# Performance work log

Hardware: AMD Instinct MI355X
Metric: run time of the kernel (lower is better)

Reference implementation:

```python
import jax, jax.numpy as jnp
import numpy as np

B, S = 256, 16384
HUBER_DELTA = 1.0  # torch.nn.HuberLoss default


def setup_inputs() -> dict:
    key = jax.random.key(0)
    k1, k2, k3 = jax.random.split(key, 3)
    pred_coords = jax.random.normal(k1, (B, S, 3), dtype=jnp.float32)
    target_coords = jax.random.normal(k2, (B, S, 3), dtype=jnp.float32)
    mask = jax.random.randint(k3, (B, S), 0, 2).astype(jnp.int32)
    return {"pred_coords": pred_coords, "target_coords": target_coords, "mask": mask}


def _kabsch_align(pred, target, maskf):
    # pred/target: [B,S,3], maskf: [B,S] (0/1). Batched masked Kabsch.
    cnt = maskf.sum(axis=1, keepdims=True)                      # [B,1]
    cp = (pred * maskf[..., None]).sum(axis=1) / cnt            # [B,3] pred center
    ct = (target * maskf[..., None]).sum(axis=1) / cnt          # [B,3] target center
    pc = (pred - cp[:, None, :]) * maskf[..., None]             # masked centered pred
    tc = target - ct[:, None, :]                                # centered target
    H = jnp.einsum('bsi,bsj->bij', pc, tc)                      # [B,3,3] covariance
    U, _, Vt = jnp.linalg.svd(H)                                # batched 3x3 SVD
    R = jnp.einsum('bji,bkj->bik', Vt, U)                       # Vt^T @ U^T
    sign = jnp.where(jnp.linalg.det(R) < 0, -1.0, 1.0)          # [B] reflection fix
    flip = jnp.ones((pred.shape[0], 3), dtype=pred.dtype).at[:, -1].set(sign)
    Vt = Vt * flip[:, :, None]                                  # flip last row of Vt
    R = jnp.einsum('bji,bkj->bik', Vt, U)
    t = ct - jnp.einsum('bij,bj->bi', R, cp)                    # [B,3]
    aligned = jnp.einsum('bij,bsj->bsi', R, pred) + t[:, None, :]
    return aligned


def _huber(d):
    a = jnp.abs(d)
    return jnp.where(a < HUBER_DELTA, 0.5 * d * d, HUBER_DELTA * (a - 0.5 * HUBER_DELTA))


def reference(pred_coords, target_coords, mask):
    maskf = mask.astype(pred_coords.dtype)                      # [B,S]
    aligned = _kabsch_align(pred_coords, target_coords, maskf)  # [B,S,3]
    # (torch computes a clamped coord_diff here but never uses it in the loss)
    loss = _huber(aligned - target_coords) * maskf[..., None]   # [B,S,3]
    return loss.sum() / maskf.sum()
```

## Files before the change

### kernel.cpp

```cpp
#include <hip/hip_runtime.h>


#define NB 256
#define NS 16384
#define TPB 256
#define PPT 4
#define CHUNKS (NS / (TPB * PPT))

__device__ __forceinline__ float wave_sum(float v) {
#pragma unroll
    for (int o = 32; o > 0; o >>= 1) v += __shfl_xor(v, o, 64);
    return v;
}

__device__ __forceinline__ float huber(float d) {
    float a = fabsf(d);
    return a < 1.f ? 0.5f * d * d : a - 0.5f;
}

__global__ __launch_bounds__(TPB) void reduce_kernel(
    const float* __restrict__ pred, const float* __restrict__ tgt,
    const int* __restrict__ mask, float* __restrict__ part)
{
    const int b = blockIdx.y, j = blockIdx.x, tid = threadIdx.x;
    const long base = (long)b * NS + (long)(j * TPB + tid) * PPT;
    const float4* p4 = reinterpret_cast<const float4*>(pred + base * 3);
    const float4* t4 = reinterpret_cast<const float4*>(tgt + base * 3);
    const int4 m4 = *reinterpret_cast<const int4*>(mask + base);
    float4 pA = p4[0], pB = p4[1], pC = p4[2];
    float4 tA = t4[0], tB = t4[1], tC = t4[2];
    float P[4][3] = {{pA.x,pA.y,pA.z},{pA.w,pB.x,pB.y},{pB.z,pB.w,pC.x},{pC.y,pC.z,pC.w}};
    float T[4][3] = {{tA.x,tA.y,tA.z},{tA.w,tB.x,tB.y},{tB.z,tB.w,tC.x},{tC.y,tC.z,tC.w}};
    float m[4] = {(float)m4.x,(float)m4.y,(float)m4.z,(float)m4.w};

    float acc[16];
#pragma unroll
    for (int i = 0; i < 16; ++i) acc[i] = 0.f;
#pragma unroll
    for (int k = 0; k < PPT; ++k) {
        const float mk = m[k];
        const float mp0 = mk * P[k][0], mp1 = mk * P[k][1], mp2 = mk * P[k][2];
        acc[0] += mk;
        acc[1] += mp0;            acc[2] += mp1;            acc[3] += mp2;
        acc[4] += mk * T[k][0];   acc[5] += mk * T[k][1];   acc[6] += mk * T[k][2];
        acc[7]  += mp0 * T[k][0]; acc[8]  += mp0 * T[k][1]; acc[9]  += mp0 * T[k][2];
        acc[10] += mp1 * T[k][0]; acc[11] += mp1 * T[k][1]; acc[12] += mp1 * T[k][2];
        acc[13] += mp2 * T[k][0]; acc[14] += mp2 * T[k][1]; acc[15] += mp2 * T[k][2];
    }
#pragma unroll
    for (int i = 0; i < 16; ++i) acc[i] = wave_sum(acc[i]);

    __shared__ float red[4][16];
    const int wave = tid >> 6, lane = tid & 63;
    if (lane == 0) {
#pragma unroll
        for (int i = 0; i < 16; ++i) red[wave][i] = acc[i];
    }
    __syncthreads();
    if (tid < 16) {
        part[((b * CHUNKS + j) << 4) + tid] =
            red[0][tid] + red[1][tid] + red[2][tid] + red[3][tid];
    }
}

__global__ __launch_bounds__(NB) void svd_kernel(
    const float* __restrict__ part, float* __restrict__ RT)
{
    const int b = threadIdx.x;
    const float4* p4 = reinterpret_cast<const float4*>(part);
    float a[16];
#pragma unroll
    for (int i = 0; i < 16; ++i) a[i] = 0.f;
    for (int k = 0; k < CHUNKS; ++k) {
        const int row = (b * CHUNKS + k) << 2;
        float4 v0 = p4[row], v1 = p4[row+1], v2 = p4[row+2], v3 = p4[row+3];
        a[0]+=v0.x;  a[1]+=v0.y;  a[2]+=v0.z;  a[3]+=v0.w;
        a[4]+=v1.x;  a[5]+=v1.y;  a[6]+=v1.z;  a[7]+=v1.w;
        a[8]+=v2.x;  a[9]+=v2.y;  a[10]+=v2.z; a[11]+=v2.w;
        a[12]+=v3.x; a[13]+=v3.y; a[14]+=v3.z; a[15]+=v3.w;
    }
    const float cnt = a[0];
    const float inv = 1.f / cnt;
    const float cpx=a[1]*inv, cpy=a[2]*inv, cpz=a[3]*inv;
    const float ctx=a[4]*inv, cty=a[5]*inv, ctz=a[6]*inv;
    const float Sxx = a[7]  - cnt*cpx*ctx;
    const float Sxy = a[8]  - cnt*cpx*cty;
    const float Sxz = a[9]  - cnt*cpx*ctz;
    const float Syx = a[10] - cnt*cpy*ctx;
    const float Syy = a[11] - cnt*cpy*cty;
    const float Syz = a[12] - cnt*cpy*ctz;
    const float Szx = a[13] - cnt*cpz*ctx;
    const float Szy = a[14] - cnt*cpz*cty;
    const float Szz = a[15] - cnt*cpz*ctz;
    const float N00 =  Sxx + Syy + Szz;
    const float N01 =  Syz - Szy;
    const float N02 =  Szx - Sxz;
    const float N03 =  Sxy - Syx;
    const float N11 =  Sxx - Syy - Szz;
    const float N12 =  Sxy + Syx;
    const float N13 =  Szx + Sxz;
    const float N22 = -Sxx + Syy - Szz;
    const float N23 =  Syz + Szy;
    const float N33 = -Sxx - Syy + Szz;
    const float fro = sqrtf(N00*N00 + N11*N11 + N22*N22 + N33*N33 +
                2.f*(N01*N01 + N02*N02 + N03*N03 + N12*N12 + N13*N13 + N23*N23));
    const float sh = fro + 1e-20f;

    float qw = 1.f, qx = 0.1f, qy = 0.2f, qz = 0.3f;
    for (int it = 0; it < 160; ++it) {
        float nw = N00*qw + N01*qx + N02*qy + N03*qz + sh*qw;
        float nx = N01*qw + N11*qx + N12*qy + N13*qz + sh*qx;
        float ny = N02*qw + N12*qx + N22*qy + N23*qz + sh*qy;
        float nz = N03*qw + N13*qx + N23*qy + N33*qz + sh*qz;
        if ((it & 3) == 3) {
            const float r = rsqrtf(nw*nw + nx*nx + ny*ny + nz*nz);
            nw *= r; nx *= r; ny *= r; nz *= r;
        }
        qw = nw; qx = nx; qy = ny; qz = nz;
    }
    {
        const float r = rsqrtf(qw*qw + qx*qx + qy*qy + qz*qz);
        qw *= r; qx *= r; qy *= r; qz *= r;
    }
    const float R00 = 1.f - 2.f*(qy*qy + qz*qz);
    const float R01 = 2.f*(qx*qy - qw*qz);
    const float R02 = 2.f*(qx*qz + qw*qy);
    const float R10 = 2.f*(qx*qy + qw*qz);
    const float R11 = 1.f - 2.f*(qx*qx + qz*qz);
    const float R12 = 2.f*(qy*qz - qw*qx);
    const float R20 = 2.f*(qx*qz - qw*qy);
    const float R21 = 2.f*(qy*qz + qw*qx);
    const float R22 = 1.f - 2.f*(qx*qx + qy*qy);
    const float tx = ctx - (R00*cpx + R01*cpy + R02*cpz);
    const float ty = cty - (R10*cpx + R11*cpy + R12*cpz);
    const float tz = ctz - (R20*cpx + R21*cpy + R22*cpz);
    float* o = RT + b * 16;
    o[0]=R00; o[1]=R01; o[2]=R02; o[3]=R10; o[4]=R11; o[5]=R12;
    o[6]=R20; o[7]=R21; o[8]=R22; o[9]=tx; o[10]=ty; o[11]=tz; o[12]=cnt;
}

__global__ __launch_bounds__(TPB) void loss_kernel(
    const float* __restrict__ pred, const float* __restrict__ tgt,
    const int* __restrict__ mask, const float* __restrict__ RT,
    float* __restrict__ lpart)
{
    const int b = blockIdx.y, j = blockIdx.x, tid = threadIdx.x;
    __shared__ float C[12];
    if (tid < 12) C[tid] = RT[b * 16 + tid];
    __syncthreads();
    const long base = (long)b * NS + (long)(j * TPB + tid) * PPT;
    const float4* p4 = reinterpret_cast<const float4*>(pred + base * 3);
    const float4* t4 = reinterpret_cast<const float4*>(tgt + base * 3);
    const int4 m4 = *reinterpret_cast<const int4*>(mask + base);
    float4 pA = p4[0], pB = p4[1], pC = p4[2];
    float4 tA = t4[0], tB = t4[1], tC = t4[2];
    float P[4][3] = {{pA.x,pA.y,pA.z},{pA.w,pB.x,pB.y},{pB.z,pB.w,pC.x},{pC.y,pC.z,pC.w}};
    float T[4][3] = {{tA.x,tA.y,tA.z},{tA.w,tB.x,tB.y},{tB.z,tB.w,tC.x},{tC.y,tC.z,tC.w}};
    float m[4] = {(float)m4.x,(float)m4.y,(float)m4.z,(float)m4.w};

    float ls = 0.f;
#pragma unroll
    for (int k = 0; k < PPT; ++k) {
        const float ax = C[0]*P[k][0] + C[1]*P[k][1] + C[2]*P[k][2] + C[9];
        const float ay = C[3]*P[k][0] + C[4]*P[k][1] + C[5]*P[k][2] + C[10];
        const float az = C[6]*P[k][0] + C[7]*P[k][1] + C[8]*P[k][2] + C[11];
        ls += m[k] * (huber(ax - T[k][0]) + huber(ay - T[k][1]) + huber(az - T[k][2]));
    }
    ls = wave_sum(ls);
    __shared__ float red[4];
    const int wave = tid >> 6, lane = tid & 63;
    if (lane == 0) red[wave] = ls;
    __syncthreads();
    if (tid == 0) lpart[b * CHUNKS + j] = red[0] + red[1] + red[2] + red[3];
}

__global__ __launch_bounds__(NB) void final_kernel(
    const float* __restrict__ lpart, const float* __restrict__ RT,
    float* __restrict__ out)
{
    const int tid = threadIdx.x;
    float ls = 0.f;
#pragma unroll
    for (int k = 0; k < CHUNKS; ++k) ls += lpart[tid + NB * k];
    float cs = RT[tid * 16 + 12];
    ls = wave_sum(ls);
    cs = wave_sum(cs);
    __shared__ float rl[4], rc[4];
    const int wave = tid >> 6, lane = tid & 63;
    if (lane == 0) { rl[wave] = ls; rc[wave] = cs; }
    __syncthreads();
    if (tid == 0)
        out[0] = (rl[0]+rl[1]+rl[2]+rl[3]) / (rc[0]+rc[1]+rc[2]+rc[3]);
}

extern "C" void kernel_launch(void* const* d_in, const int* in_sizes, int n_in,
                              void* d_out, int out_size, void* d_ws, size_t ws_size,
                              hipStream_t stream) {
    const float* pred = (const float*)d_in[0];
    const float* tgt  = (const float*)d_in[1];
    const int*   mask = (const int*)d_in[2];
    float* out = (float*)d_out;

    float* part  = (float*)d_ws;
    float* RT    = part + NB * CHUNKS * 16;
    float* lpart = RT + NB * 16;

    dim3 grid(CHUNKS, NB);
    reduce_kernel<<<grid, TPB, 0, stream>>>(pred, tgt, mask, part);
    svd_kernel<<<1, NB, 0, stream>>>(part, RT);
    loss_kernel<<<grid, TPB, 0, stream>>>(pred, tgt, mask, RT, lpart);
    final_kernel<<<1, NB, 0, stream>>>(lpart, RT, out);
}
```

Measured before the change: 169.0 us.

## Fuse final reduction into loss kernel via atomics and halve block count

```diff
diff --git a/kernel.cpp b/kernel.cpp
--- a/kernel.cpp
+++ b/kernel.cpp
@@ -4,8 +4,10 @@
 #define NB 256
 #define NS 16384
 #define TPB 256
+#define PB 8
+#define SUB 2
 #define PPT 4
-#define CHUNKS (NS / (TPB * PPT))
+#define NBLK (NB * PB)
 
 __device__ __forceinline__ float wave_sum(float v) {
 #pragma unroll
@@ -20,32 +22,36 @@
 
 __global__ __launch_bounds__(TPB) void reduce_kernel(
     const float* __restrict__ pred, const float* __restrict__ tgt,
-    const int* __restrict__ mask, float* __restrict__ part)
+    const int* __restrict__ mask, float* __restrict__ part,
+    float* __restrict__ lsum, unsigned* __restrict__ counter)
 {
     const int b = blockIdx.y, j = blockIdx.x, tid = threadIdx.x;
-    const long base = (long)b * NS + (long)(j * TPB + tid) * PPT;
-    const float4* p4 = reinterpret_cast<const float4*>(pred + base * 3);
-    const float4* t4 = reinterpret_cast<const float4*>(tgt + base * 3);
-    const int4 m4 = *reinterpret_cast<const int4*>(mask + base);
-    float4 pA = p4[0], pB = p4[1], pC = p4[2];
-    float4 tA = t4[0], tB = t4[1], tC = t4[2];
-    float P[4][3] = {{pA.x,pA.y,pA.z},{pA.w,pB.x,pB.y},{pB.z,pB.w,pC.x},{pC.y,pC.z,pC.w}};
-    float T[4][3] = {{tA.x,tA.y,tA.z},{tA.w,tB.x,tB.y},{tB.z,tB.w,tC.x},{tC.y,tC.z,tC.w}};
-    float m[4] = {(float)m4.x,(float)m4.y,(float)m4.z,(float)m4.w};
-
     float acc[16];
 #pragma unroll
     for (int i = 0; i < 16; ++i) acc[i] = 0.f;
 #pragma unroll
-    for (int k = 0; k < PPT; ++k) {
-        const float mk = m[k];
-        const float mp0 = mk * P[k][0], mp1 = mk * P[k][1], mp2 = mk * P[k][2];
-        acc[0] += mk;
-        acc[1] += mp0;            acc[2] += mp1;            acc[3] += mp2;
-        acc[4] += mk * T[k][0];   acc[5] += mk * T[k][1];   acc[6] += mk * T[k][2];
-        acc[7]  += mp0 * T[k][0]; acc[8]  += mp0 * T[k][1]; acc[9]  += mp0 * T[k][2];
-        acc[10] += mp1 * T[k][0]; acc[11] += mp1 * T[k][1]; acc[12] += mp1 * T[k][2];
-        acc[13] += mp2 * T[k][0]; acc[14] += mp2 * T[k][1]; acc[15] += mp2 * T[k][2];
+    for (int c = 0; c < SUB; ++c) {
+        const long base = (long)b * NS + (long)j * (SUB * TPB * PPT)
+                        + (long)c * (TPB * PPT) + (long)tid * PPT;
+        const float4* p4 = reinterpret_cast<const float4*>(pred + base * 3);
+        const float4* t4 = reinterpret_cast<const float4*>(tgt + base * 3);
+        const int4 m4 = *reinterpret_cast<const int4*>(mask + base);
+        float4 pA = p4[0], pB = p4[1], pC = p4[2];
+        float4 tA = t4[0], tB = t4[1], tC = t4[2];
+        float P[4][3] = {{pA.x,pA.y,pA.z},{pA.w,pB.x,pB.y},{pB.z,pB.w,pC.x},{pC.y,pC.z,pC.w}};
+        float T[4][3] = {{tA.x,tA.y,tA.z},{tA.w,tB.x,tB.y},{tB.z,tB.w,tC.x},{tC.y,tC.z,tC.w}};
+        float m[4] = {(float)m4.x,(float)m4.y,(float)m4.z,(float)m4.w};
+#pragma unroll
+        for (int k = 0; k < PPT; ++k) {
+            const float mk = m[k];
+            const float mp0 = mk * P[k][0], mp1 = mk * P[k][1], mp2 = mk * P[k][2];
+            acc[0] += mk;
+            acc[1] += mp0;            acc[2] += mp1;            acc[3] += mp2;
+            acc[4] += mk * T[k][0];   acc[5] += mk * T[k][1];   acc[6] += mk * T[k][2];
+            acc[7]  += mp0 * T[k][0]; acc[8]  += mp0 * T[k][1]; acc[9]  += mp0 * T[k][2];
+            acc[10] += mp1 * T[k][0]; acc[11] += mp1 * T[k][1]; acc[12] += mp1 * T[k][2];
+            acc[13] += mp2 * T[k][0]; acc[14] += mp2 * T[k][1]; acc[15] += mp2 * T[k][2];
+        }
     }
 #pragma unroll
     for (int i = 0; i < 16; ++i) acc[i] = wave_sum(acc[i]);
@@ -57,22 +63,24 @@
         for (int i = 0; i < 16; ++i) red[wave][i] = acc[i];
     }
     __syncthreads();
-    if (tid < 16) {
-        part[((b * CHUNKS + j) << 4) + tid] =
+    if (tid < 16)
+        part[((b * PB + j) << 4) + tid] =
             red[0][tid] + red[1][tid] + red[2][tid] + red[3][tid];
-    }
+    if (b == 0 && j == 0 && tid == 0) { *lsum = 0.f; *counter = 0u; }
 }
 
 __global__ __launch_bounds__(NB) void svd_kernel(
-    const float* __restrict__ part, float* __restrict__ RT)
+    const float* __restrict__ part, float* __restrict__ RT,
+    float* __restrict__ totc)
 {
     const int b = threadIdx.x;
     const float4* p4 = reinterpret_cast<const float4*>(part);
     float a[16];
 #pragma unroll
     for (int i = 0; i < 16; ++i) a[i] = 0.f;
-    for (int k = 0; k < CHUNKS; ++k) {
-        const int row = (b * CHUNKS + k) << 2;
+#pragma unroll
+    for (int k = 0; k < PB; ++k) {
+        const int row = (b * PB + k) << 2;
         float4 v0 = p4[row], v1 = p4[row+1], v2 = p4[row+2], v3 = p4[row+3];
         a[0]+=v0.x;  a[1]+=v0.y;  a[2]+=v0.z;  a[3]+=v0.w;
         a[4]+=v1.x;  a[5]+=v1.y;  a[6]+=v1.z;  a[7]+=v1.w;
@@ -92,36 +100,36 @@
     const float Szx = a[13] - cnt*cpz*ctx;
     const float Szy = a[14] - cnt*cpz*cty;
     const float Szz = a[15] - cnt*cpz*ctz;
-    const float N00 =  Sxx + Syy + Szz;
-    const float N01 =  Syz - Szy;
-    const float N02 =  Szx - Sxz;
-    const float N03 =  Sxy - Syx;
-    const float N11 =  Sxx - Syy - Szz;
-    const float N12 =  Sxy + Syx;
-    const float N13 =  Szx + Sxz;
-    const float N22 = -Sxx + Syy - Szz;
-    const float N23 =  Syz + Szy;
-    const float N33 = -Sxx - Syy + Szz;
+    float N00 =  Sxx + Syy + Szz;
+    float N01 =  Syz - Szy;
+    float N02 =  Szx - Sxz;
+    float N03 =  Sxy - Syx;
+    float N11 =  Sxx - Syy - Szz;
+    float N12 =  Sxy + Syx;
+    float N13 =  Szx + Sxz;
+    float N22 = -Sxx + Syy - Szz;
+    float N23 =  Syz + Szy;
+    float N33 = -Sxx - Syy + Szz;
     const float fro = sqrtf(N00*N00 + N11*N11 + N22*N22 + N33*N33 +
                 2.f*(N01*N01 + N02*N02 + N03*N03 + N12*N12 + N13*N13 + N23*N23));
-    const float sh = fro + 1e-20f;
+    const float isc = 1.f / (fro + 1e-30f);
+    N00*=isc; N01*=isc; N02*=isc; N03*=isc; N11*=isc;
+    N12*=isc; N13*=isc; N22*=isc; N23*=isc; N33*=isc;
 
     float qw = 1.f, qx = 0.1f, qy = 0.2f, qz = 0.3f;
     for (int it = 0; it < 160; ++it) {
-        float nw = N00*qw + N01*qx + N02*qy + N03*qz + sh*qw;
-        float nx = N01*qw + N11*qx + N12*qy + N13*qz + sh*qx;
-        float ny = N02*qw + N12*qx + N22*qy + N23*qz + sh*qy;
-        float nz = N03*qw + N13*qx + N23*qy + N33*qz + sh*qz;
-        if ((it & 3) == 3) {
+        float nw = N00*qw + N01*qx + N02*qy + N03*qz + qw;
+        float nx = N01*qw + N11*qx + N12*qy + N13*qz + qx;
+        float ny = N02*qw + N12*qx + N22*qy + N23*qz + qy;
+        float nz = N03*qw + N13*qx + N23*qy + N33*qz + qz;
+        if ((it & 7) == 7) {
             const float r = rsqrtf(nw*nw + nx*nx + ny*ny + nz*nz);
             nw *= r; nx *= r; ny *= r; nz *= r;
         }
         qw = nw; qx = nx; qy = ny; qz = nz;
     }
-    {
-        const float r = rsqrtf(qw*qw + qx*qx + qy*qy + qz*qz);
-        qw *= r; qx *= r; qy *= r; qz *= r;
-    }
+    const float r = rsqrtf(qw*qw + qx*qx + qy*qy + qz*qz);
+    qw *= r; qx *= r; qy *= r; qz *= r;
     const float R00 = 1.f - 2.f*(qy*qy + qz*qz);
     const float R01 = 2.f*(qx*qy - qw*qz);
     const float R02 = 2.f*(qx*qz + qw*qy);
@@ -131,66 +139,69 @@
     const float R20 = 2.f*(qx*qz - qw*qy);
     const float R21 = 2.f*(qy*qz + qw*qx);
     const float R22 = 1.f - 2.f*(qx*qx + qy*qy);
-    const float tx = ctx - (R00*cpx + R01*cpy + R02*cpz);
-    const float ty = cty - (R10*cpx + R11*cpy + R12*cpz);
-    const float tz = ctz - (R20*cpx + R21*cpy + R22*cpz);
     float* o = RT + b * 16;
     o[0]=R00; o[1]=R01; o[2]=R02; o[3]=R10; o[4]=R11; o[5]=R12;
-    o[6]=R20; o[7]=R21; o[8]=R22; o[9]=tx; o[10]=ty; o[11]=tz; o[12]=cnt;
+    o[6]=R20; o[7]=R21; o[8]=R22;
+    o[9]  = ctx - (R00*cpx + R01*cpy + R02*cpz);
+    o[10] = cty - (R10*cpx + R11*cpy + R12*cpz);
+    o[11] = ctz - (R20*cpx + R21*cpy + R22*cpz);
+    o[12] = cnt;
+
+    float tc = wave_sum(cnt);
+    __shared__ float rc[4];
+    const int wave = b >> 6, lane = b & 63;
+    if (lane == 0) rc[wave] = tc;
+    __syncthreads();
+    if (b == 0) *totc = rc[0] + rc[1] + rc[2] + rc[3];
 }
 
 __global__ __launch_bounds__(TPB) void loss_kernel(
     const float* __restrict__ pred, const float* __restrict__ tgt,
     const int* __restrict__ mask, const float* __restrict__ RT,
-    float* __restrict__ lpart)
+    const float* __restrict__ totc, float* __restrict__ lsum,
+    unsigned* __restrict__ counter, float* __restrict__ out)
 {
     const int b = blockIdx.y, j = blockIdx.x, tid = threadIdx.x;
     __shared__ float C[12];
     if (tid < 12) C[tid] = RT[b * 16 + tid];
     __syncthreads();
-    const long base = (long)b * NS + (long)(j * TPB + tid) * PPT;
-    const float4* p4 = reinterpret_cast<const float4*>(pred + base * 3);
-    const float4* t4 = reinterpret_cast<const float4*>(tgt + base * 3);
-    const int4 m4 = *reinterpret_cast<const int4*>(mask + base);
-    float4 pA = p4[0], pB = p4[1], pC = p4[2];
-    float4 tA = t4[0], tB = t4[1], tC = t4[2];
-    float P[4][3] = {{pA.x,pA.y,pA.z},{pA.w,pB.x,pB.y},{pB.z,pB.w,pC.x},{pC.y,pC.z,pC.w}};
-    float T[4][3] = {{tA.x,tA.y,tA.z},{tA.w,tB.x,tB.y},{tB.z,tB.w,tC.x},{tC.y,tC.z,tC.w}};
-    float m[4] = {(float)m4.x,(float)m4.y,(float)m4.z,(float)m4.w};
-
     float ls = 0.f;
 #pragma unroll
-    for (int k = 0; k < PPT; ++k) {
-        const float ax = C[0]*P[k][0] + C[1]*P[k][1] + C[2]*P[k][2] + C[9];
-        const float ay = C[3]*P[k][0] + C[4]*P[k][1] + C[5]*P[k][2] + C[10];
-        const float az = C[6]*P[k][0] + C[7]*P[k][1] + C[8]*P[k][2] + C[11];
-        ls += m[k] * (huber(ax - T[k][0]) + huber(ay - T[k][1]) + huber(az - T[k][2]));
+    for (int c = 0; c < SUB; ++c) {
+        const long base = (long)b * NS + (long)j * (SUB * TPB * PPT)
+                        + (long)c * (TPB * PPT) + (long)tid * PPT;
+        const float4* p4 = reinterpret_cast<const float4*>(pred + base * 3);
+        const float4* t4 = reinterpret_cast<const float4*>(tgt + base * 3);
+        const int4 m4 = *reinterpret_cast<const int4*>(mask + base);
+        float4 pA = p4[0], pB = p4[1], pC = p4[2];
+        float4 tA = t4[0], tB = t4[1], tC = t4[2];
+        float P[4][3] = {{pA.x,pA.y,pA.z},{pA.w,pB.x,pB.y},{pB.z,pB.w,pC.x},{pC.y,pC.z,pC.w}};
+        float T[4][3] = {{tA.x,tA.y,tA.z},{tA.w,tB.x,tB.y},{tB.z,tB.w,tC.x},{tC.y,tC.z,tC.w}};
+        float m[4] = {(float)m4.x,(float)m4.y,(float)m4.z,(float)m4.w};
+#pragma unroll
+        for (int k = 0; k < PPT; ++k) {
+            const float ax = C[0]*P[k][0] + C[1]*P[k][1] + C[2]*P[k][2] + C[9];
+            const float ay = C[3]*P[k][0] + C[4]*P[k][1] + C[5]*P[k][2] + C[10];
+            const float az = C[6]*P[k][0] + C[7]*P[k][1] + C[8]*P[k][2] + C[11];
+            ls += m[k] * (huber(ax - T[k][0]) + huber(ay - T[k][1]) + huber(az - T[k][2]));
+        }
     }
     ls = wave_sum(ls);
     __shared__ float red[4];
     const int wave = tid >> 6, lane = tid & 63;
     if (lane == 0) red[wave] = ls;
     __syncthreads();
-    if (tid == 0) lpart[b * CHUNKS + j] = red[0] + red[1] + red[2] + red[3];
-}
-
-__global__ __launch_bounds__(NB) void final_kernel(
-    const float* __restrict__ lpart, const float* __restrict__ RT,
-    float* __restrict__ out)
-{
-    const int tid = threadIdx.x;
-    float ls = 0.f;
-#pragma unroll
-    for (int k = 0; k < CHUNKS; ++k) ls += lpart[tid + NB * k];
-    float cs = RT[tid * 16 + 12];
-    ls = wave_sum(ls);
-    cs = wave_sum(cs);
-    __shared__ float rl[4], rc[4];
-    const int wave = tid >> 6, lane = tid & 63;
-    if (lane == 0) { rl[wave] = ls; rc[wave] = cs; }
-    __syncthreads();
-    if (tid == 0)
-        out[0] = (rl[0]+rl[1]+rl[2]+rl[3]) / (rc[0]+rc[1]+rc[2]+rc[3]);
+    if (tid == 0) {
+        const float blk = red[0] + red[1] + red[2] + red[3];
+        atomicAdd(lsum, blk);
+        __threadfence();
+        const unsigned old = atomicAdd(counter, 1u);
+        if (old == NBLK - 1) {
+            __threadfence();
+            const float total = atomicAdd(lsum, 0.f);
+            out[0] = total / *totc;
+        }
+    }
 }
 
 extern "C" void kernel_launch(void* const* d_in, const int* in_sizes, int n_in,
@@ -201,13 +212,14 @@
     const int*   mask = (const int*)d_in[2];
     float* out = (float*)d_out;
 
-    float* part  = (float*)d_ws;
-    float* RT    = part + NB * CHUNKS * 16;
-    float* lpart = RT + NB * 16;
-
-    dim3 grid(CHUNKS, NB);
-    reduce_kernel<<<grid, TPB, 0, stream>>>(pred, tgt, mask, part);
-    svd_kernel<<<1, NB, 0, stream>>>(part, RT);
-    loss_kernel<<<grid, TPB, 0, stream>>>(pred, tgt, mask, RT, lpart);
-    final_kernel<<<1, NB, 0, stream>>>(lpart, RT, out);
-}
+    float* part = (float*)d_ws;
+    float* RT   = part + NBLK * 16;
+    float* totc = RT + NB * 16;
+    float* lsum = totc + 1;
+    unsigned* counter = (unsigned*)(lsum + 1);
+
+    dim3 grid(PB, NB);
+    reduce_kernel<<<grid, TPB, 0, stream>>>(pred, tgt, mask, part, lsum, counter);
+    svd_kernel<<<1, NB, 0, stream>>>(part, RT, totc);
+    loss_kernel<<<grid, TPB, 0, stream>>>(pred, tgt, mask, RT, totc, lsum, counter, out);
+}
```

After: 230.1 us. +36.2%, slower.
